# Performance work log

Hardware: AMD Instinct MI355X
Metric: run time of the kernel (lower is better)

The kernel has to match this reference:

```python
import jax, jax.numpy as jnp
import numpy as np

N_NODES = 100000


def setup_inputs() -> dict:
    key = jax.random.key(0)
    k1, k2, k3 = jax.random.split(key, 3)
    x = jax.random.normal(k1, (N_NODES, 256), dtype=jnp.float32)
    edge_index = jax.random.randint(k2, (2, 1600000), 0, N_NODES, dtype=jnp.int64)
    W = jax.random.normal(k3, (256, 128), dtype=jnp.float32) * (1.0 / np.sqrt(256.0))
    b = jnp.zeros((128,), dtype=jnp.float32)
    alpha = jnp.full((128,), 0.25, dtype=jnp.float32)  # PReLU default init
    return {"x": x, "edge_index": edge_index, "W": W, "b": b, "alpha": alpha}


def reference(x, edge_index, W, b, alpha):
    N = x.shape[0]
    # --- GCNConv: add self-loops ---
    loops = jnp.arange(N, dtype=edge_index.dtype)
    row = jnp.concatenate([edge_index[0], loops])  # source nodes
    col = jnp.concatenate([edge_index[1], loops])  # destination nodes
    # symmetric normalization: deg computed at destinations (self-loops => deg >= 1)
    deg = jax.ops.segment_sum(jnp.ones(col.shape, x.dtype), col, num_segments=N)
    dinv = jax.lax.rsqrt(deg)
    norm = dinv[row] * dinv[col]  # [E+N]
    # linear transform then normalized scatter-add aggregation
    h = x @ W  # [N, H]
    msg = h[row] * norm[:, None]  # [E+N, H]
    out = jax.ops.segment_sum(msg, col, num_segments=N) + b  # bias after aggregation
    # --- PReLU (per-channel) ---
    return jnp.where(out >= 0, out, alpha * out)
```

## Files before the change

### kernel.cpp

```cpp
#include <hip/hip_runtime.h>

constexpr int KDIM  = 256;
constexpr int HDIM  = 128;
constexpr int BK    = 128;
constexpr int CHUNK = 8192;
constexpr int NBMAX = 800;

typedef __bf16 bf16x8 __attribute__((ext_vector_type(8)));
typedef float  f32x4  __attribute__((ext_vector_type(4)));

__device__ __forceinline__ ushort f2bf(float f) {
    unsigned u = __float_as_uint(f);
    unsigned r = (u + 0x7fffu + ((u >> 16) & 1u)) >> 16;
    return (ushort)r;
}

__device__ __forceinline__ void accum8(float* a, uint4 u) {
    a[0] += __uint_as_float(u.x << 16); a[1] += __uint_as_float(u.x & 0xffff0000u);
    a[2] += __uint_as_float(u.y << 16); a[3] += __uint_as_float(u.y & 0xffff0000u);
    a[4] += __uint_as_float(u.z << 16); a[5] += __uint_as_float(u.z & 0xffff0000u);
    a[6] += __uint_as_float(u.w << 16); a[7] += __uint_as_float(u.w & 0xffff0000u);
}

__global__ __launch_bounds__(256) void prep_sort_kernel(
    const float* __restrict__ W, ushort* __restrict__ Wt, ushort* __restrict__ hsb,
    const int* __restrict__ row, const int* __restrict__ col,
    uint* __restrict__ ebuf, int* __restrict__ histG, int* __restrict__ localOff,
    int n, int e, int nbv, int gblk) {
    int b = blockIdx.x, t = threadIdx.x;
    if (b < 16) {
        int g = b * 256 + t;
        int lane = g & 63, cn = g >> 6;
        int c = cn >> 3, nf = cn & 7;
        int ncol = nf * 16 + (lane & 15);
        int k0 = c * 32 + (lane >> 4) * 8;
        ushort* dst = Wt + (size_t)g * 8;
        #pragma unroll
        for (int j = 0; j < 8; ++j) dst[j] = f2bf(W[(k0 + j) * HDIM + ncol]);
        return;
    }
    if (b == 16) {
        if (t < HDIM) hsb[(size_t)n * HDIM + t] = 0;
        return;
    }
    int g = b - 17;
    __shared__ uint dst[CHUNK];
    __shared__ int hist[NBMAX], excl[NBMAX], cur[NBMAX];
    __shared__ int ws2[4];
    int lane = t & 63, w = t >> 6;
    for (int i = t; i < nbv; i += 256) hist[i] = 0;
    __syncthreads();
    int lo = g * CHUNK, hi = min(lo + CHUNK, e);
    for (int i = lo + t; i < hi; i += 256)
        atomicAdd(&hist[col[i] >> 7], 1);
    __syncthreads();
    {
        int b0 = t * 4;
        int h[4]; int s = 0;
        #pragma unroll
        for (int j = 0; j < 4; ++j) { h[j] = (b0 + j < nbv) ? hist[b0 + j] : 0; s += h[j]; }
        int incl = s;
        #pragma unroll
        for (int d = 1; d < 64; d <<= 1) { int u = __shfl_up(incl, d, 64); if (lane >= d) incl += u; }
        if (lane == 63) ws2[w] = incl;
        __syncthreads();
        int add = 0;
        #pragma unroll
        for (int i = 0; i < 4; ++i) if (i < w) add += ws2[i];
        int run = add + incl - s;
        #pragma unroll
        for (int j = 0; j < 4; ++j) {
            if (b0 + j < nbv) { excl[b0 + j] = run; cur[b0 + j] = run; }
            run += h[j];
        }
    }
    __syncthreads();
    for (int i = lo + t; i < hi; i += 256) {
        int c = col[i];
        int bk = c >> 7;
        int p = atomicAdd(&cur[bk], 1);
        dst[p] = ((uint)row[i] << 7) | (uint)(c & 127);
    }
    __syncthreads();
    int cnt = hi - lo;
    for (int i = t; i < cnt; i += 256) ebuf[lo + i] = dst[i];
    for (int i = t; i < nbv; i += 256) {
        histG[i * gblk + g]    = hist[i];
        localOff[i * gblk + g] = excl[i];
    }
}

__global__ __launch_bounds__(256) void scanA_kernel(const int* __restrict__ in,
                                                    int* __restrict__ partial, int n) {
    int t = threadIdx.x, base = blockIdx.x * 1024;
    int s = 0;
    #pragma unroll
    for (int j = 0; j < 4; ++j) {
        int i = base + j * 256 + t;
        if (i < n) s += in[i];
    }
    __shared__ int ws[4];
    #pragma unroll
    for (int d = 1; d < 64; d <<= 1) s += __shfl_xor(s, d, 64);
    int lane = t & 63, w = t >> 6;
    if (lane == 0) ws[w] = s;
    __syncthreads();
    if (t == 0) partial[blockIdx.x] = ws[0] + ws[1] + ws[2] + ws[3];
}

__global__ void scanB_kernel(int* __restrict__ partial, int nb) {
    int t = threadIdx.x;
    int v = (t < nb) ? partial[t] : 0;
    int orig = v;
    int lane = t & 63, w = t >> 6;
    #pragma unroll
    for (int d = 1; d < 64; d <<= 1) { int u = __shfl_up(v, d, 64); if (lane >= d) v += u; }
    __shared__ int ws[4];
    if (lane == 63) ws[w] = v;
    __syncthreads();
    int add = 0;
    #pragma unroll
    for (int i = 0; i < 4; ++i) if (i < w) add += ws[i];
    if (t < nb) partial[t] = v + add - orig;
}

__global__ __launch_bounds__(256) void scanC_kernel(const int* __restrict__ in,
                                                    const int* __restrict__ partial,
                                                    int* __restrict__ out, int n) {
    int t = threadIdx.x, base = blockIdx.x * 1024;
    int vals[4], tsum = 0;
    #pragma unroll
    for (int j = 0; j < 4; ++j) {
        int i = base + t * 4 + j;
        vals[j] = (i < n) ? in[i] : 0;
        tsum += vals[j];
    }
    int lane = t & 63, w = t >> 6;
    int incl = tsum;
    #pragma unroll
    for (int d = 1; d < 64; d <<= 1) { int u = __shfl_up(incl, d, 64); if (lane >= d) incl += u; }
    __shared__ int ws[4];
    if (lane == 63) ws[w] = incl;
    __syncthreads();
    int add = partial[blockIdx.x];
    #pragma unroll
    for (int i = 0; i < 4; ++i) if (i < w) add += ws[i];
    int run = add + incl - tsum;
    #pragma unroll
    for (int j = 0; j < 4; ++j) {
        int i = base + t * 4 + j;
        if (i < n) out[i] = run;
        run += vals[j];
    }
}

__global__ __launch_bounds__(256) void fine_kernel(const uint* __restrict__ ebuf,
                                                   const int* __restrict__ histG,
                                                   const int* __restrict__ localOff,
                                                   const int* __restrict__ histS,
                                                   uint* __restrict__ csr,
                                                   int* __restrict__ deg,
                                                   int* __restrict__ offs,
                                                   float* __restrict__ dinv,
                                                   int e, int nbv, int gblk, int n) {
    __shared__ uint elist[4096];
    __shared__ uint csrl[4096];
    __shared__ int hist[BK], excl[BK], cur[BK];
    int b = blockIdx.x, t = threadIdx.x;
    int seg0 = histS[b * gblk];
    int seg1 = (b + 1 < nbv) ? histS[(b + 1) * gblk] : e;
    int cnt = min(seg1 - seg0, 4096);

    if (t < BK) { hist[t] = 0; cur[t] = 0; }
    for (int g = t; g < gblk; g += 256) {
        int c   = histG[b * gblk + g];
        int src = g * CHUNK + localOff[b * gblk + g];
        int dst = histS[b * gblk + g] - seg0;
        for (int i = 0; i < c; ++i) elist[dst + i] = ebuf[src + i];
    }
    __syncthreads();
    for (int i = t; i < cnt; i += 256) atomicAdd(&hist[elist[i] & 127], 1);
    __syncthreads();
    if (t < 64) {
        int v0 = hist[2 * t], v1 = hist[2 * t + 1];
        int s = v0 + v1, incl = s;
        #pragma unroll
        for (int d = 1; d < 64; d <<= 1) { int u = __shfl_up(incl, d, 64); if (t >= d) incl += u; }
        int base = incl - s;
        excl[2 * t] = base; excl[2 * t + 1] = base + v0;
    }
    __syncthreads();
    for (int i = t; i < cnt; i += 256) {
        uint v = elist[i];
        int d = v & 127;
        int r = atomicAdd(&cur[d], 1);
        csrl[excl[d] + r] = v >> 7;
    }
    __syncthreads();
    for (int i = t; i < cnt; i += 256) csr[seg0 + i] = csrl[i];
    if (t < BK) {
        int node = b * BK + t;
        if (node < n) {
            int dg = hist[t];
            deg[node]  = dg;
            offs[node] = seg0 + excl[t];
            dinv[node] = rsqrtf((float)(dg + 1));
        }
    }
}


constexpr int MT = 64;
constexpr int XS_STRIDE = 264;

__global__ __launch_bounds__(256) void gemm_kernel(const float* __restrict__ x,
                                                   const ushort* __restrict__ Wt,
                                                   const float* __restrict__ dinv,
                                                   ushort* __restrict__ hsb, int n) {
    __shared__ ushort xs[MT * XS_STRIDE];
    __shared__ float sdinv[MT];
    int t = threadIdx.x, lane = t & 63, w = t >> 6;
    int row0 = blockIdx.x * MT;

    bf16x8 bfrag[8][2];
    #pragma unroll
    for (int c = 0; c < 8; ++c)
        #pragma unroll
        for (int f = 0; f < 2; ++f)
            bfrag[c][f] = *(const bf16x8*)(Wt + (size_t)(((c * 8) + (w * 2 + f)) * 64 + lane) * 8);

    #pragma unroll
    for (int i = 0; i < 16; ++i) {
        int rl = w * 16 + i;
        int gr = row0 + rl; if (gr >= n) gr = n - 1;
        float4 v = *(const float4*)(x + (size_t)gr * KDIM + lane * 4);
        ushort4 o;
        o.x = f2bf(v.x); o.y = f2bf(v.y); o.z = f2bf(v.z); o.w = f2bf(v.w);
        *(ushort4*)(xs + rl * XS_STRIDE + lane * 4) = o;
    }
    if (t < MT) { int g = row0 + t; sdinv[t] = dinv[(g < n) ? g : (n - 1)]; }
    __syncthreads();

    #pragma unroll
    for (int s = 0; s < MT / 16; ++s) {
        f32x4 acc0 = {0.f, 0.f, 0.f, 0.f}, acc1 = {0.f, 0.f, 0.f, 0.f};
        #pragma unroll
        for (int c = 0; c < 8; ++c) {
            const ushort* ap = xs + (s * 16 + (lane & 15)) * XS_STRIDE + c * 32 + (lane >> 4) * 8;
            bf16x8 afrag = *(const bf16x8*)ap;
            acc0 = __builtin_amdgcn_mfma_f32_16x16x32_bf16(afrag, bfrag[c][0], acc0, 0, 0, 0);
            acc1 = __builtin_amdgcn_mfma_f32_16x16x32_bf16(afrag, bfrag[c][1], acc1, 0, 0, 0);
        }
        #pragma unroll
        for (int reg = 0; reg < 4; ++reg) {
            int rl = s * 16 + (lane >> 4) * 4 + reg;
            int gr = row0 + rl;
            if (gr < n) {
                float d = sdinv[rl];
                int col0 = w * 32 + (lane & 15);
                hsb[(size_t)gr * HDIM + col0]      = f2bf(acc0[reg] * d);
                hsb[(size_t)gr * HDIM + col0 + 16] = f2bf(acc1[reg] * d);
            }
        }
    }
}


__global__ __launch_bounds__(256) void aggregate_kernel(
    const ushort* __restrict__ hsb, const int* __restrict__ offs,
    const int* __restrict__ deg, const int* __restrict__ csr,
    const float* __restrict__ dinv, const float* __restrict__ b,
    const float* __restrict__ alpha, float* __restrict__ out, int n) {
    int wv = threadIdx.x >> 6, lane = threadIdx.x & 63;
    int node = blockIdx.x * 4 + wv;
    if (node >= n) return;
    int base = offs[node], cnt = deg[node];
    int slot = lane >> 4, chg = lane & 15;
    const uint4* hs4 = (const uint4*)hsb;

    float a[8];
    #pragma unroll
    for (int i = 0; i < 8; ++i) a[i] = 0.f;

    if (slot == 0) {
        uint4 u = hs4[(size_t)node * 16 + chg];
        accum8(a, u);
    }

    for (int j = 0; j < cnt; j += 64) {
        int m = min(cnt - j, 64);
        int idx = (lane < m) ? (int)csr[base + j + lane] : n;
        for (int g = 0; g < m; g += 16) {
            int s0 = __shfl(idx, g + slot, 64);
            int s1 = __shfl(idx, g + 4 + slot, 64);
            int s2 = __shfl(idx, g + 8 + slot, 64);
            int s3 = __shfl(idx, g + 12 + slot, 64);
            uint4 u0 = hs4[(size_t)s0 * 16 + chg];
            uint4 u1 = hs4[(size_t)s1 * 16 + chg];
            uint4 u2 = hs4[(size_t)s2 * 16 + chg];
            uint4 u3 = hs4[(size_t)s3 * 16 + chg];
            accum8(a, u0); accum8(a, u1); accum8(a, u2); accum8(a, u3);
        }
    }

    #pragma unroll
    for (int i = 0; i < 8; ++i) {
        a[i] += __shfl_xor(a[i], 16, 64);
        a[i] += __shfl_xor(a[i], 32, 64);
    }

    if (slot == 0) {
        float dc = dinv[node];
        int c0 = chg * 8;
        float o[8];
        #pragma unroll
        for (int i = 0; i < 8; ++i) {
            float v = fmaf(dc, a[i], b[c0 + i]);
            o[i] = v >= 0.f ? v : alpha[c0 + i] * v;
        }
        float* op = out + (size_t)node * HDIM + c0;
        *(float4*)op       = make_float4(o[0], o[1], o[2], o[3]);
        *(float4*)(op + 4) = make_float4(o[4], o[5], o[6], o[7]);
    }
}


extern "C" void kernel_launch(void* const* d_in, const int* in_sizes, int n_in,
                              void* d_out, int out_size, void* d_ws, size_t ws_size,
                              hipStream_t stream) {
    const float* x     = (const float*)d_in[0];
    const int*   ei    = (const int*)d_in[1];
    const float* W     = (const float*)d_in[2];
    const float* b     = (const float*)d_in[3];
    const float* alpha = (const float*)d_in[4];
    float* out = (float*)d_out;

    int E = in_sizes[1] / 2;
    int N = in_sizes[0] / KDIM;
    int NB = (N + BK - 1) / BK;
    int GBLK = (E + CHUNK - 1) / CHUNK;
    int SCAN_N = NB * GBLK;

    ushort* hsb   = (ushort*)d_ws;
    ushort* Wt    = hsb + (size_t)(N + 1) * HDIM;
    float* dinv   = (float*)(Wt + 32768);
    int* deg      = (int*)(dinv + N);
    int* offs     = deg + N;
    int* histG    = offs + N;
    int* localOff = histG + SCAN_N;
    int* histS    = localOff + SCAN_N;
    int* partial  = histS + SCAN_N;
    uint* ebuf    = (uint*)(partial + 512);
    uint* csr     = ebuf + (size_t)GBLK * CHUNK;

    const int* rowp = ei;
    const int* colp = ei + E;

    int nbScan = (SCAN_N + 1023) / 1024;

    hipLaunchKernelGGL(prep_sort_kernel, dim3(17 + GBLK), dim3(256), 0, stream,
                       W, Wt, hsb, rowp, colp, ebuf, histG, localOff, N, E, NB, GBLK);
    hipLaunchKernelGGL(scanA_kernel, dim3(nbScan), dim3(256), 0, stream, histG, partial, SCAN_N);
    hipLaunchKernelGGL(scanB_kernel, dim3(1), dim3(256), 0, stream, partial, nbScan);
    hipLaunchKernelGGL(scanC_kernel, dim3(nbScan), dim3(256), 0, stream, histG, partial, histS, SCAN_N);
    hipLaunchKernelGGL(fine_kernel, dim3(NB), dim3(256), 0, stream,
                       ebuf, histG, localOff, histS, csr, deg, offs, dinv, E, NB, GBLK, N);
    hipLaunchKernelGGL(gemm_kernel, dim3((N + MT - 1) / MT), dim3(256), 0, stream, x, Wt, dinv, hsb, N);
    hipLaunchKernelGGL(aggregate_kernel, dim3((N + 3) / 4), dim3(256), 0, stream,
                       hsb, offs, deg, (const int*)csr, dinv, b, alpha, out, N);
}
```

Baseline: 334.0 us.

## Map one node per 16-lane group in aggregation and vectorize the sort prep

```diff
diff --git a/kernel.cpp b/kernel.cpp
--- a/kernel.cpp
+++ b/kernel.cpp
@@ -22,69 +22,104 @@
     a[6] += __uint_as_float(u.w << 16); a[7] += __uint_as_float(u.w & 0xffff0000u);
 }
 
-__global__ __launch_bounds__(256) void prep_sort_kernel(
+__global__ __launch_bounds__(512) void prep_sort_kernel(
     const float* __restrict__ W, ushort* __restrict__ Wt, ushort* __restrict__ hsb,
     const int* __restrict__ row, const int* __restrict__ col,
     uint* __restrict__ ebuf, int* __restrict__ histG, int* __restrict__ localOff,
     int n, int e, int nbv, int gblk) {
+    __shared__ uint dst[CHUNK];
+    __shared__ int hist[NBMAX], excl[NBMAX], cur[NBMAX];
+    __shared__ int ws2[8];
     int b = blockIdx.x, t = threadIdx.x;
-    if (b < 16) {
-        int g = b * 256 + t;
+    if (b < 8) {
+        int g = b * 512 + t;
         int lane = g & 63, cn = g >> 6;
         int c = cn >> 3, nf = cn & 7;
         int ncol = nf * 16 + (lane & 15);
         int k0 = c * 32 + (lane >> 4) * 8;
-        ushort* dst = Wt + (size_t)g * 8;
-        #pragma unroll
-        for (int j = 0; j < 8; ++j) dst[j] = f2bf(W[(k0 + j) * HDIM + ncol]);
+        ushort* dp = Wt + (size_t)g * 8;
+        #pragma unroll
+        for (int j = 0; j < 8; ++j) dp[j] = f2bf(W[(k0 + j) * HDIM + ncol]);
         return;
     }
-    if (b == 16) {
+    if (b == 8) {
         if (t < HDIM) hsb[(size_t)n * HDIM + t] = 0;
         return;
     }
-    int g = b - 17;
-    __shared__ uint dst[CHUNK];
-    __shared__ int hist[NBMAX], excl[NBMAX], cur[NBMAX];
-    __shared__ int ws2[4];
+    int g = b - 9;
     int lane = t & 63, w = t >> 6;
-    for (int i = t; i < nbv; i += 256) hist[i] = 0;
+    for (int i = t; i < nbv; i += 512) hist[i] = 0;
     __syncthreads();
     int lo = g * CHUNK, hi = min(lo + CHUNK, e);
-    for (int i = lo + t; i < hi; i += 256)
-        atomicAdd(&hist[col[i] >> 7], 1);
+    int colr[16];
+    #pragma unroll
+    for (int k = 0; k < 4; ++k) {
+        int i0 = lo + (k * 512 + t) * 4;
+        if (i0 + 3 < hi) {
+            int4 c4 = *(const int4*)(col + i0);
+            colr[k * 4 + 0] = c4.x; colr[k * 4 + 1] = c4.y;
+            colr[k * 4 + 2] = c4.z; colr[k * 4 + 3] = c4.w;
+            atomicAdd(&hist[c4.x >> 7], 1); atomicAdd(&hist[c4.y >> 7], 1);
+            atomicAdd(&hist[c4.z >> 7], 1); atomicAdd(&hist[c4.w >> 7], 1);
+        } else {
+            #pragma unroll
+            for (int j = 0; j < 4; ++j) {
+                int i = i0 + j;
+                int c = (i < hi) ? col[i] : -1;
+                colr[k * 4 + j] = c;
+                if (c >= 0) atomicAdd(&hist[c >> 7], 1);
+            }
+        }
+    }
     __syncthreads();
     {
-        int b0 = t * 4;
-        int h[4]; int s = 0;
-        #pragma unroll
-        for (int j = 0; j < 4; ++j) { h[j] = (b0 + j < nbv) ? hist[b0 + j] : 0; s += h[j]; }
-        int incl = s;
+        int b0 = t * 2;
+        int h0 = (b0 < nbv) ? hist[b0] : 0;
+        int h1 = (b0 + 1 < nbv) ? hist[b0 + 1] : 0;
+        int s = h0 + h1, incl = s;
         #pragma unroll
         for (int d = 1; d < 64; d <<= 1) { int u = __shfl_up(incl, d, 64); if (lane >= d) incl += u; }
         if (lane == 63) ws2[w] = incl;
         __syncthreads();
         int add = 0;
         #pragma unroll
-        for (int i = 0; i < 4; ++i) if (i < w) add += ws2[i];
+        for (int i = 0; i < 8; ++i) if (i < w) add += ws2[i];
         int run = add + incl - s;
-        #pragma unroll
-        for (int j = 0; j < 4; ++j) {
-            if (b0 + j < nbv) { excl[b0 + j] = run; cur[b0 + j] = run; }
-            run += h[j];
-        }
-    }
-    __syncthreads();
-    for (int i = lo + t; i < hi; i += 256) {
-        int c = col[i];
-        int bk = c >> 7;
-        int p = atomicAdd(&cur[bk], 1);
-        dst[p] = ((uint)row[i] << 7) | (uint)(c & 127);
+        if (b0 < nbv)     { excl[b0] = run;          cur[b0] = run; }
+        if (b0 + 1 < nbv) { excl[b0 + 1] = run + h0; cur[b0 + 1] = run + h0; }
+    }
+    __syncthreads();
+    #pragma unroll
+    for (int k = 0; k < 4; ++k) {
+        int i0 = lo + (k * 512 + t) * 4;
+        if (i0 + 3 < hi) {
+            int4 r4 = *(const int4*)(row + i0);
+            int rr[4] = {r4.x, r4.y, r4.z, r4.w};
+            #pragma unroll
+            for (int j = 0; j < 4; ++j) {
+                int c = colr[k * 4 + j];
+                int p = atomicAdd(&cur[c >> 7], 1);
+                dst[p] = ((uint)rr[j] << 7) | (uint)(c & 127);
+            }
+        } else {
+            #pragma unroll
+            for (int j = 0; j < 4; ++j) {
+                int i = i0 + j, c = colr[k * 4 + j];
+                if (c >= 0) {
+                    int p = atomicAdd(&cur[c >> 7], 1);
+                    dst[p] = ((uint)row[i] << 7) | (uint)(c & 127);
+                }
+            }
+        }
     }
     __syncthreads();
     int cnt = hi - lo;
-    for (int i = t; i < cnt; i += 256) ebuf[lo + i] = dst[i];
-    for (int i = t; i < nbv; i += 256) {
+    for (int k = 0; k < 4; ++k) {
+        int i0 = (k * 512 + t) * 4;
+        if (i0 + 3 < cnt) *(uint4*)(ebuf + lo + i0) = *(uint4*)&dst[i0];
+        else for (int j = 0; j < 4; ++j) if (i0 + j < cnt) ebuf[lo + i0 + j] = dst[i0 + j];
+    }
+    for (int i = t; i < nbv; i += 512) {
         histG[i * gblk + g]    = hist[i];
         localOff[i * gblk + g] = excl[i];
     }
@@ -272,46 +307,37 @@
     const float* __restrict__ dinv, const float* __restrict__ b,
     const float* __restrict__ alpha, float* __restrict__ out, int n) {
     int wv = threadIdx.x >> 6, lane = threadIdx.x & 63;
-    int node = blockIdx.x * 4 + wv;
-    if (node >= n) return;
-    int base = offs[node], cnt = deg[node];
-    int slot = lane >> 4, chg = lane & 15;
+    int grp = lane >> 4, li = lane & 15;
+    int node = blockIdx.x * 16 + wv * 4 + grp;
+    bool valid = node < n;
+    int nd   = valid ? node : n;
+    int base = valid ? offs[node] : 0;
+    int cnt  = valid ? deg[node] : 0;
     const uint4* hs4 = (const uint4*)hsb;
 
     float a[8];
     #pragma unroll
     for (int i = 0; i < 8; ++i) a[i] = 0.f;
 
-    if (slot == 0) {
-        uint4 u = hs4[(size_t)node * 16 + chg];
-        accum8(a, u);
-    }
-
-    for (int j = 0; j < cnt; j += 64) {
-        int m = min(cnt - j, 64);
-        int idx = (lane < m) ? (int)csr[base + j + lane] : n;
-        for (int g = 0; g < m; g += 16) {
-            int s0 = __shfl(idx, g + slot, 64);
-            int s1 = __shfl(idx, g + 4 + slot, 64);
-            int s2 = __shfl(idx, g + 8 + slot, 64);
-            int s3 = __shfl(idx, g + 12 + slot, 64);
-            uint4 u0 = hs4[(size_t)s0 * 16 + chg];
-            uint4 u1 = hs4[(size_t)s1 * 16 + chg];
-            uint4 u2 = hs4[(size_t)s2 * 16 + chg];
-            uint4 u3 = hs4[(size_t)s3 * 16 + chg];
-            accum8(a, u0); accum8(a, u1); accum8(a, u2); accum8(a, u3);
-        }
-    }
-
-    #pragma unroll
-    for (int i = 0; i < 8; ++i) {
-        a[i] += __shfl_xor(a[i], 16, 64);
-        a[i] += __shfl_xor(a[i], 32, 64);
-    }
-
-    if (slot == 0) {
+    uint4 su = hs4[(size_t)nd * 16 + li];
+    accum8(a, su);
+
+    for (int it = 0; it < cnt; it += 4) {
+        int src_l = (li < 4 && (it + li) < cnt) ? (int)csr[base + it + li] : n;
+        int s0 = __shfl(src_l, grp * 16 + 0, 64);
+        int s1 = __shfl(src_l, grp * 16 + 1, 64);
+        int s2 = __shfl(src_l, grp * 16 + 2, 64);
+        int s3 = __shfl(src_l, grp * 16 + 3, 64);
+        uint4 u0 = hs4[(size_t)s0 * 16 + li];
+        uint4 u1 = hs4[(size_t)s1 * 16 + li];
+        uint4 u2 = hs4[(size_t)s2 * 16 + li];
+        uint4 u3 = hs4[(size_t)s3 * 16 + li];
+        accum8(a, u0); accum8(a, u1); accum8(a, u2); accum8(a, u3);
+    }
+
+    if (valid) {
         float dc = dinv[node];
-        int c0 = chg * 8;
+        int c0 = li * 8;
         float o[8];
         #pragma unroll
         for (int i = 0; i < 8; ++i) {
@@ -358,7 +384,7 @@
 
     int nbScan = (SCAN_N + 1023) / 1024;
 
-    hipLaunchKernelGGL(prep_sort_kernel, dim3(17 + GBLK), dim3(256), 0, stream,
+    hipLaunchKernelGGL(prep_sort_kernel, dim3(9 + GBLK), dim3(512), 0, stream,
                        W, Wt, hsb, rowp, colp, ebuf, histG, localOff, N, E, NB, GBLK);
     hipLaunchKernelGGL(scanA_kernel, dim3(nbScan), dim3(256), 0, stream, histG, partial, SCAN_N);
     hipLaunchKernelGGL(scanB_kernel, dim3(1), dim3(256), 0, stream, partial, nbScan);
@@ -366,6 +392,6 @@
     hipLaunchKernelGGL(fine_kernel, dim3(NB), dim3(256), 0, stream,
                        ebuf, histG, localOff, histS, csr, deg, offs, dinv, E, NB, GBLK, N);
     hipLaunchKernelGGL(gemm_kernel, dim3((N + MT - 1) / MT), dim3(256), 0, stream, x, Wt, dinv, hsb, N);
-    hipLaunchKernelGGL(aggregate_kernel, dim3((N + 3) / 4), dim3(256), 0, stream,
+    hipLaunchKernelGGL(aggregate_kernel, dim3((N + 15) / 16), dim3(256), 0, stream,
                        hsb, offs, deg, (const int*)csr, dinv, b, alpha, out, N);
 }
```

Result: faster. 296.2 us (-11.3%).
